# Optimization experiments

Measured on AMD Instinct MI355X. Metric: run time of the kernel, lower is better.

## Reference

```python
import jax, jax.numpy as jnp
import numpy as np

N = 100000
E = 400000
G = 2000  # number of graphs in batch
IN_DIM = 32
H = 192
L = 4
EPS = 1e-5


def setup_inputs() -> dict:
    key = jax.random.key(0)
    ks = jax.random.split(key, 20)
    x = jax.random.normal(ks[0], (N, IN_DIM), jnp.float32)
    edge_src = jax.random.randint(ks[1], (E,), 0, N, jnp.int32)
    edge_dst = jax.random.randint(ks[2], (E,), 0, N, jnp.int32)
    batch = jnp.sort(jax.random.randint(ks[3], (N,), 0, G, jnp.int32))
    s_in = 1.0 / np.sqrt(IN_DIM)
    s_h = 1.0 / np.sqrt(H)
    return {
        "x": x,
        "edge_src": edge_src,
        "edge_dst": edge_dst,
        "batch": batch,
        # layer 0 (in_dim -> H); weights stored [in, out]
        "Wrel0": jax.random.uniform(ks[4], (IN_DIM, H), jnp.float32, -s_in, s_in),
        "brel0": jax.random.uniform(ks[5], (H,), jnp.float32, -s_in, s_in),
        "Wroot0": jax.random.uniform(ks[6], (IN_DIM, H), jnp.float32, -s_in, s_in),
        # layers 1..3 stacked (H -> H)
        "Wrel": jax.random.uniform(ks[7], (L - 1, H, H), jnp.float32, -s_h, s_h),
        "brel": jax.random.uniform(ks[8], (L - 1, H), jnp.float32, -s_h, s_h),
        "Wroot": jax.random.uniform(ks[9], (L - 1, H, H), jnp.float32, -s_h, s_h),
        # batchnorm affine params for all 4 layers
        "gamma": jnp.ones((L, H), jnp.float32),
        "beta": jnp.zeros((L, H), jnp.float32),
        # head MLP and output
        "Wh1": jax.random.uniform(ks[10], (H, H), jnp.float32, -s_h, s_h),
        "bh1": jax.random.uniform(ks[11], (H,), jnp.float32, -s_h, s_h),
        "Wh2": jax.random.uniform(ks[12], (H, H), jnp.float32, -s_h, s_h),
        "bh2": jax.random.uniform(ks[13], (H,), jnp.float32, -s_h, s_h),
        "Wout": jax.random.uniform(ks[14], (H, 1), jnp.float32, -s_h, s_h),
        "bout": jax.random.uniform(ks[15], (1,), jnp.float32, -s_h, s_h),
    }


def _rel_conv(x, edge_src, edge_dst, Wrel, brel, Wroot):
    # message: lin_rel(x_j); applying the linear at node level first is the
    # same math as per-edge (linear commutes with gather) and cheaper.
    h = x @ Wrel + brel                      # [N, out]
    agg = jax.ops.segment_sum(h[edge_src], edge_dst, num_segments=N)
    return agg + x @ Wroot


def _bn_relu(h, g, b):
    # BatchNorm1d in training mode: batch stats over node dim, biased var
    mu = h.mean(axis=0)
    var = jnp.var(h, axis=0)
    h = (h - mu) * jax.lax.rsqrt(var + EPS) * g + b
    return jax.nn.relu(h)


def reference(x, edge_src, edge_dst, batch, Wrel0, brel0, Wroot0,
              Wrel, brel, Wroot, gamma, beta, Wh1, bh1, Wh2, bh2, Wout, bout):
    h = _bn_relu(_rel_conv(x, edge_src, edge_dst, Wrel0, brel0, Wroot0),
                 gamma[0], beta[0])
    for i in range(L - 1):
        h = _bn_relu(_rel_conv(h, edge_src, edge_dst, Wrel[i], brel[i], Wroot[i]),
                     gamma[i + 1], beta[i + 1])
    # global mean pool over graphs
    sums = jax.ops.segment_sum(h, batch, num_segments=G)          # [G, H]
    cnt = jax.ops.segment_sum(jnp.ones((N,), h.dtype), batch, num_segments=G)
    g = sums / jnp.maximum(cnt, 1.0)[:, None]
    # head MLP (dropout is identity at eval) + output linear
    g = jax.nn.relu(g @ Wh1 + bh1) @ Wh2 + bh2
    return g @ Wout + bout                                        # [G, 1]
```

## Files before the change

kernel.cpp:

```cpp
#include <hip/hip_runtime.h>

#define HDIM 192
#define EPS 1e-5f

typedef __attribute__((ext_vector_type(8))) _Float16 half8;
typedef __attribute__((ext_vector_type(4))) float floatx4;

__device__ __forceinline__ float h2f(ushort u) {
    union { ushort u; _Float16 h; } c; c.u = u; return (float)c.h;
}
__device__ __forceinline__ ushort f2h(float x) {
    _Float16 h = (_Float16)x;
    union { _Float16 h; ushort u; } c; c.h = h; return c.u;
}
__device__ __forceinline__ uint4 pack8(const ushort* h) {
    uint4 p;
    p.x = h[0] | ((uint)h[1] << 16); p.y = h[2] | ((uint)h[3] << 16);
    p.z = h[4] | ((uint)h[5] << 16); p.w = h[6] | ((uint)h[7] << 16);
    return p;
}

__device__ __forceinline__ void gload_lds16(const ushort* g, ushort* l) {
    __builtin_amdgcn_global_load_lds(
        (const __attribute__((address_space(1))) unsigned int*)g,
        (__attribute__((address_space(3))) unsigned int*)l, 16, 0, 0);
}

#define WAITV0() asm volatile("s_waitcnt vmcnt(0)" ::: "memory")


struct PrepArgs {
    const float* src[6];
    ushort*      dst[6];
    int K[6];
    int off[7];
};

__global__ __launch_bounds__(256) void prep_all_k(PrepArgs a)
{
    int idx = blockIdx.x * 256 + threadIdx.x;
    if (idx >= a.off[6]) return;
    int i = 0;
    #pragma unroll
    for (int t = 1; t < 6; ++t) if (idx >= a.off[t]) i = t;
    int r = idx - a.off[i];
    int K = a.K[i];
    int perMat = (K >> 5) * 12 * 64;
    int mat = r / perMat;
    r -= mat * perMat;
    int lane = r & 63;
    int ct = (r >> 6) % 12;
    int kc = r / (12 * 64);
    int col = ct * 16 + (lane & 15);
    int kb  = kc * 32 + (lane >> 4) * 8;
    const float* Wm = a.src[i] + (size_t)mat * K * HDIM;
    ushort* base = a.dst[i] + (size_t)mat * K * HDIM;
    size_t o = (size_t)kc * 6144 + (size_t)(ct * 64 + lane) * 8;
    #pragma unroll
    for (int j = 0; j < 8; ++j)
        base[o + j] = f2h(Wm[(size_t)(kb + j) * HDIM + col]);
}

__global__ __launch_bounds__(256) void conv_half_k(
    const float* __restrict__ src, ushort* __restrict__ dst, int R, int C)
{
    int OC = C >> 3;
    int idx = blockIdx.x * 256 + threadIdx.x;
    if (idx >= R * OC) return;
    int r = idx / OC;
    int o = idx - r * OC;
    float4 v0 = ((const float4*)(src + (size_t)r * C + o * 8))[0];
    float4 v1 = ((const float4*)(src + (size_t)r * C + o * 8))[1];
    float v[8] = {v0.x, v0.y, v0.z, v0.w, v1.x, v1.y, v1.z, v1.w};
    ushort h[8];
    #pragma unroll
    for (int t = 0; t < 8; ++t) h[t] = f2h(v[t]);
    *(uint4*)(dst + (size_t)r * C + o * 8) = pack8(h);
}

template<bool DUAL, bool RELU, bool DEG, bool STATS, int NKC>
__global__ __launch_bounds__(256, 3) void gemm_mfma_k(
    const ushort* __restrict__ A1h, const ushort* __restrict__ W1f,
    const ushort* __restrict__ A2h, const ushort* __restrict__ W2f,
    const float* __restrict__ degf, const float* __restrict__ bias,
    ushort* __restrict__ C, float* __restrict__ pstats, int N, int K)
{
    constexpr int KR   = NKC * 32;
    constexpr int RS   = KR + 8;
    constexpr int SLAB = 64 * RS;
    constexpr int NINSTR = SLAB / 512;
    constexpr int NCH  = DUAL ? 2 * NKC : NKC;
    constexpr int SMEMU = ((DUAL ? 2 * SLAB : SLAB) > 12800)
                            ? (DUAL ? 2 * SLAB : SLAB) : 12800;

    __shared__ float sstat[2][HDIM];
    __shared__ __align__(16) ushort smem[SMEMU];
    const int tid  = threadIdx.x;
    const int wave = tid >> 6;
    const int lane = tid & 63;
    const int row0 = blockIdx.x * 64;
    const int m16 = lane & 15;
    const int g4  = lane >> 4;

    if (STATS && tid < HDIM) { sstat[0][tid] = 0.f; sstat[1][tid] = 0.f; }

    auto stage = [&](const ushort* Ab, int slabOff) {
        #pragma unroll
        for (int i = wave; i < NINSTR; i += 4) {
            int slotB = i * 1024 + lane * 16;
            int r   = slotB / (RS * 2);
            int off = slotB - r * (RS * 2);
            if (off >= KR * 2) off = KR * 2 - 16;
            int rr = row0 + r; if (rr >= N) rr = N - 1;
            gload_lds16(Ab + (size_t)rr * KR + (off >> 1),
                        smem + slabOff + i * 512);
        }
    };

    stage(A1h, 0);
    if constexpr (DUAL) stage(A2h, SLAB);
    WAITV0();
    __builtin_amdgcn_s_barrier();
    __builtin_amdgcn_sched_barrier(0);

    auto loadB = [&](int c, half8* b) {
        bool ph = DUAL && (c >= NKC);
        int kc = ph ? c - NKC : c;
        const ushort* Bp = (ph ? W2f : W1f) + (size_t)kc * 6144
                         + (size_t)(wave * 192 + lane) * 8;
        #pragma unroll
        for (int ct = 0; ct < 3; ++ct)
            b[ct] = *(const half8*)(Bp + ct * 512);
    };

    floatx4 acc[4][3];
    #pragma unroll
    for (int s = 0; s < 4; ++s)
        #pragma unroll
        for (int ct = 0; ct < 3; ++ct) acc[s][ct] = (floatx4){0.f, 0.f, 0.f, 0.f};

    half8 bA[3], bB[3];
    loadB(0, bA);
    #pragma unroll
    for (int c = 0; c < NCH; ++c) {
        if (c + 1 < NCH) loadB(c + 1, (c & 1) ? bA : bB);
        const int base = (DUAL && c >= NKC) ? SLAB : 0;
        const int kc   = (DUAL && c >= NKC) ? c - NKC : c;
        const ushort* aB = smem + base + m16 * RS + kc * 32 + g4 * 8;
        half8 a[4];
        #pragma unroll
        for (int s = 0; s < 4; ++s)
            a[s] = *(const half8*)(aB + s * 16 * RS);
        const half8* bu = (c & 1) ? bB : bA;
        #pragma unroll
        for (int ct = 0; ct < 3; ++ct)
            #pragma unroll
            for (int s = 0; s < 4; ++s)
                acc[s][ct] = __builtin_amdgcn_mfma_f32_16x16x32_f16(a[s], bu[ct], acc[s][ct], 0, 0, 0);
    }

    __syncthreads();
    #pragma unroll
    for (int ct = 0; ct < 3; ++ct) {
        int col = wave * 48 + ct * 16 + m16;
        float bv = bias ? bias[col] : 0.f;
        float lsum = 0.f, lsq = 0.f;
        #pragma unroll
        for (int s = 0; s < 4; ++s) {
            #pragma unroll
            for (int reg = 0; reg < 4; ++reg) {
                int rloc = s * 16 + g4 * 4 + reg;
                int rr = row0 + rloc;
                int rrc = rr < N ? rr : N - 1;
                float v = acc[s][ct][reg] + (DEG ? degf[rrc] * bv : bv);
                if (STATS && rr < N) { lsum += v; lsq += v * v; }
                if (RELU) v = fmaxf(v, 0.f);
                smem[rloc * 200 + col] = f2h(v);
            }
        }
        if (STATS) {
            lsum += __shfl_xor(lsum, 16); lsum += __shfl_xor(lsum, 32);
            lsq  += __shfl_xor(lsq, 16);  lsq  += __shfl_xor(lsq, 32);
            if (g4 == 0) {
                atomicAdd(&sstat[0][col], lsum);
                atomicAdd(&sstat[1][col], lsq);
            }
        }
    }
    __syncthreads();
    {
        int rowsLeft = N - row0; if (rowsLeft > 64) rowsLeft = 64;
        int lim = rowsLeft * 24;
        ushort* Cb = C + (size_t)row0 * HDIM;
        #pragma unroll
        for (int k = 0; k < 6; ++k) {
            int u = tid + k * 256;
            if (u < lim) {
                int r  = u / 24;
                int c8 = (u - r * 24) * 8;
                *(uint4*)(Cb + (size_t)u * 8) =
                    *(const uint4*)(smem + r * 200 + c8);
            }
        }
    }
    if (STATS) {
        if (tid < HDIM) {
            float* pb = pstats + (size_t)blockIdx.x * (2 * HDIM);
            pb[tid]        = sstat[0][tid];
            pb[HDIM + tid] = sstat[1][tid];
        }
    }
}

__global__ __launch_bounds__(512, 4) void gemm_fused_k(
    const ushort* __restrict__ Hraw, const ushort* __restrict__ W1f,
    const ushort* __restrict__ W2f,
    const float* __restrict__ degf, const float* __restrict__ bias,
    const float* __restrict__ instats, const float* __restrict__ gammaL,
    const float* __restrict__ betaL, float invN,
    const int* __restrict__ row_ptr, const int* __restrict__ col,
    ushort* __restrict__ C, float* __restrict__ pstats, int N)
{
    constexpr int KR   = 192;
    constexpr int RS   = 200;
    constexpr int SLAB = 64 * RS;
    constexpr int NINSTR = SLAB / 512;
    constexpr int NKC  = 6, NCH = 12;

    __shared__ float sstat[2][HDIM];
    __shared__ __align__(16) ushort smem[2 * SLAB];
    const int tid  = threadIdx.x;
    const int wave = tid >> 6;
    const int lane = tid & 63;
    const int row0 = blockIdx.x * 64;
    const int m16 = lane & 15;
    const int g4  = lane >> 4;

    #pragma unroll
    for (int i = wave; i < NINSTR; i += 8) {
        int slotB = i * 1024 + lane * 16;
        int r   = slotB / (RS * 2);
        int off = slotB - r * (RS * 2);
        if (off >= KR * 2) off = KR * 2 - 16;
        int rr = row0 + r; if (rr >= N) rr = N - 1;
        gload_lds16(Hraw + (size_t)rr * KR + (off >> 1),
                    smem + SLAB + i * 512);
    }
    WAITV0();
    __builtin_amdgcn_s_barrier();
    __builtin_amdgcn_sched_barrier(0);

    if (tid < HDIM) {
        float mu  = instats[tid] * invN;
        float var = instats[HDIM + tid] * invN - mu * mu;
        float s = gammaL[tid] * rsqrtf(var + EPS);
        sstat[0][tid] = s;
        sstat[1][tid] = betaL[tid] - mu * s;
    }
    __syncthreads();

    const int r  = tid >> 3;
    const int q8 = tid & 7;
    {
        ushort* rowp = smem + SLAB + r * RS + q8 * 24;
        #pragma unroll
        for (int k = 0; k < 3; ++k) {
            uint4 hv = *(uint4*)(rowp + k * 8);
            uint hu[4] = {hv.x, hv.y, hv.z, hv.w};
            ushort oh[8];
            #pragma unroll
            for (int e = 0; e < 4; ++e) {
                int ch = q8 * 24 + k * 8 + e * 2;
                float v0 = h2f((ushort)(hu[e] & 0xffffu)) * sstat[0][ch]     + sstat[1][ch];
                float v1 = h2f((ushort)(hu[e] >> 16))     * sstat[0][ch + 1] + sstat[1][ch + 1];
                oh[2*e]   = f2h(fmaxf(v0, 0.f));
                oh[2*e+1] = f2h(fmaxf(v1, 0.f));
            }
            *(uint4*)(rowp + k * 8) = pack8(oh);
        }
    }
    {
        float acc[24];
        #pragma unroll
        for (int i = 0; i < 24; ++i) acc[i] = 0.f;
        int rr = row0 + r;
        if (rr < N) {
            int j0 = row_ptr[rr], j1 = row_ptr[rr + 1];
            const ushort* hp = Hraw + q8 * 24;
            for (int j = j0; j < j1; ++j) {
                int s = col[j];
                const ushort* rp = hp + (size_t)s * KR;
                uint4 h0 = *(const uint4*)(rp);
                uint4 h1 = *(const uint4*)(rp + 8);
                uint4 h2 = *(const uint4*)(rp + 16);
                uint hu[12] = {h0.x,h0.y,h0.z,h0.w, h1.x,h1.y,h1.z,h1.w,
                               h2.x,h2.y,h2.z,h2.w};
                #pragma unroll
                for (int e = 0; e < 12; ++e) {
                    int ch = q8 * 24 + e * 2;
                    float v0 = h2f((ushort)(hu[e] & 0xffffu)) * sstat[0][ch]     + sstat[1][ch];
                    float v1 = h2f((ushort)(hu[e] >> 16))     * sstat[0][ch + 1] + sstat[1][ch + 1];
                    acc[e*2]     += fmaxf(v0, 0.f);
                    acc[e*2 + 1] += fmaxf(v1, 0.f);
                }
            }
        }
        ushort* dst = smem + r * RS + q8 * 24;
        #pragma unroll
        for (int ck = 0; ck < 3; ++ck) {
            ushort oh[8];
            #pragma unroll
            for (int e = 0; e < 8; ++e) oh[e] = f2h(acc[ck*8 + e]);
            *(uint4*)(dst + ck * 8) = pack8(oh);
        }
    }
    __syncthreads();
    if (tid < HDIM) { sstat[0][tid] = 0.f; sstat[1][tid] = 0.f; }

    const int rg = wave >> 2;
    const int cg = wave & 3;

    auto loadB = [&](int c, half8* b) {
        bool ph = (c >= NKC);
        int kc = ph ? c - NKC : c;
        const ushort* Bp = (ph ? W2f : W1f) + (size_t)kc * 6144
                         + (size_t)(cg * 192 + lane) * 8;
        #pragma unroll
        for (int ct = 0; ct < 3; ++ct)
            b[ct] = *(const half8*)(Bp + ct * 512);
    };

    floatx4 acc[2][3];
    #pragma unroll
    for (int s = 0; s < 2; ++s)
        #pragma unroll
        for (int ct = 0; ct < 3; ++ct) acc[s][ct] = (floatx4){0.f, 0.f, 0.f, 0.f};

    half8 bA[3], bB[3];
    loadB(0, bA);
    #pragma unroll
    for (int c = 0; c < NCH; ++c) {
        if (c + 1 < NCH) loadB(c + 1, (c & 1) ? bA : bB);
        const int base = (c >= NKC) ? SLAB : 0;
        const int kc   = (c >= NKC) ? c - NKC : c;
        const ushort* aB = smem + base + (rg * 32 + m16) * RS + kc * 32 + g4 * 8;
        half8 a[2];
        #pragma unroll
        for (int s = 0; s < 2; ++s)
            a[s] = *(const half8*)(aB + s * 16 * RS);
        const half8* bu = (c & 1) ? bB : bA;
        #pragma unroll
        for (int ct = 0; ct < 3; ++ct)
            #pragma unroll
            for (int s = 0; s < 2; ++s)
                acc[s][ct] = __builtin_amdgcn_mfma_f32_16x16x32_f16(a[s], bu[ct], acc[s][ct], 0, 0, 0);
    }

    __syncthreads();
    #pragma unroll
    for (int ct = 0; ct < 3; ++ct) {
        int colc = cg * 48 + ct * 16 + m16;
        float bv = bias[colc];
        float lsum = 0.f, lsq = 0.f;
        #pragma unroll
        for (int s = 0; s < 2; ++s) {
            #pragma unroll
            for (int reg = 0; reg < 4; ++reg) {
                int rloc = rg * 32 + s * 16 + g4 * 4 + reg;
                int rr = row0 + rloc;
                int rrc = rr < N ? rr : N - 1;
                float v = acc[s][ct][reg] + degf[rrc] * bv;
                if (rr < N) { lsum += v; lsq += v * v; }
                smem[rloc * 200 + colc] = f2h(v);
            }
        }
        lsum += __shfl_xor(lsum, 16); lsum += __shfl_xor(lsum, 32);
        lsq  += __shfl_xor(lsq, 16);  lsq  += __shfl_xor(lsq, 32);
        if (g4 == 0) {
            atomicAdd(&sstat[0][colc], lsum);
            atomicAdd(&sstat[1][colc], lsq);
        }
    }
    __syncthreads();
    {
        int rowsLeft = N - row0; if (rowsLeft > 64) rowsLeft = 64;
        int lim = rowsLeft * 24;
        ushort* Cb = C + (size_t)row0 * HDIM;
        #pragma unroll
        for (int k = 0; k < 3; ++k) {
            int u = tid + k * 512;
            if (u < lim) {
                int rr = u / 24;
                int c8 = (u - rr * 24) * 8;
                *(uint4*)(Cb + (size_t)u * 8) =
                    *(const uint4*)(smem + rr * 200 + c8);
            }
        }
    }
    if (tid < HDIM) {
        float* pb = pstats + (size_t)blockIdx.x * (2 * HDIM);
        pb[tid]        = sstat[0][tid];
        pb[HDIM + tid] = sstat[1][tid];
    }
}

__global__ __launch_bounds__(256) void bn_reduce_k(
    const float* __restrict__ pbuf, float* __restrict__ stats, int nb)
{
    __shared__ float red[32][9];
    int t  = threadIdx.x;
    int cl = t & 7;
    int s  = t >> 3;
    int c  = blockIdx.x * 8 + cl;
    float acc = 0.f;
    int b = s;
    for (; b + 96 < nb; b += 128) {
        float a0 = pbuf[(size_t)b * 384 + c];
        float a1 = pbuf[(size_t)(b + 32) * 384 + c];
        float a2 = pbuf[(size_t)(b + 64) * 384 + c];
        float a3 = pbuf[(size_t)(b + 96) * 384 + c];
        acc += a0 + a1 + a2 + a3;
    }
    for (; b < nb; b += 32)
        acc += pbuf[(size_t)b * 384 + c];
    red[s][cl] = acc;
    __syncthreads();
    if (t < 8) {
        float a = 0.f;
        #pragma unroll
        for (int i = 0; i < 32; ++i) a += red[i][t];
        stats[blockIdx.x * 8 + t] = a;
    }
}

__global__ __launch_bounds__(256) void hist_k(
    const int* __restrict__ dst, int* __restrict__ deg, int E)
{
    int e = blockIdx.x * 256 + threadIdx.x;
    if (e < E) atomicAdd(&deg[dst[e]], 1);
}

__global__ __launch_bounds__(256) void block_sum_k(
    const int* __restrict__ deg, int* __restrict__ bsum, int N)
{
    __shared__ int s[256];
    int t = threadIdx.x;
    int n = blockIdx.x * 256 + t;
    s[t] = (n < N) ? deg[n] : 0;
    __syncthreads();
    for (int off = 128; off > 0; off >>= 1) {
        if (t < off) s[t] += s[t + off];
        __syncthreads();
    }
    if (t == 0) bsum[blockIdx.x] = s[0];
}

__global__ __launch_bounds__(512) void scan_bsum_k(int* __restrict__ bsum, int nb)
{
    __shared__ int s[512];
    int t = threadIdx.x;
    int v = (t < nb) ? bsum[t] : 0;
    s[t] = v;
    __syncthreads();
    for (int off = 1; off < 512; off <<= 1) {
        int u = (t >= off) ? s[t - off] : 0;
        __syncthreads();
        s[t] += u;
        __syncthreads();
    }
    if (t < nb) bsum[t] = s[t] - v;
}

__global__ __launch_bounds__(256) void row_ptr_k(
    const int* __restrict__ deg, const int* __restrict__ bsum,
    int* __restrict__ row_ptr, int* __restrict__ cursor,
    float* __restrict__ degf, int N, int E)
{
    __shared__ int s[256];
    int t = threadIdx.x;
    int n = blockIdx.x * 256 + t;
    int v = (n < N) ? deg[n] : 0;
    s[t] = v;
    __syncthreads();
    for (int off = 1; off < 256; off <<= 1) {
        int u = (t >= off) ? s[t - off] : 0;
        __syncthreads();
        s[t] += u;
        __syncthreads();
    }
    int ex = s[t] - v + bsum[blockIdx.x];
    if (n < N) {
        row_ptr[n] = ex;
        cursor[n]  = ex;
        degf[n]    = (float)v;
    }
    if (blockIdx.x == 0 && t == 0) row_ptr[N] = E;
}

__global__ __launch_bounds__(256) void fill_k(
    const int* __restrict__ src, const int* __restrict__ dst,
    int* __restrict__ cursor, int* __restrict__ col, int E)
{
    int e = blockIdx.x * 256 + threadIdx.x;
    if (e < E) {
        int p = atomicAdd(&cursor[dst[e]], 1);
        col[p] = src[e];
    }
}

__global__ __launch_bounds__(256) void gather_h_k(
    const ushort* __restrict__ xh, const int* __restrict__ row_ptr,
    const int* __restrict__ col, ushort* __restrict__ gh, int N, int K)
{
    int OC = K >> 3;
    int idx = blockIdx.x * 256 + threadIdx.x;
    if (idx >= N * OC) return;
    int n = idx / OC;
    int o = idx - n * OC;
    const ushort* hp = xh + o * 8;
    int j0 = row_ptr[n], j1 = row_ptr[n + 1];
    float acc[8] = {0.f,0.f,0.f,0.f,0.f,0.f,0.f,0.f};
    auto addrow = [&](uint4 hv) {
        uint hu[4] = {hv.x, hv.y, hv.z, hv.w};
        #pragma unroll
        for (int t = 0; t < 4; ++t) {
            acc[2*t]   += h2f((ushort)(hu[t] & 0xffffu));
            acc[2*t+1] += h2f((ushort)(hu[t] >> 16));
        }
    };
    int j = j0;
    for (; j + 3 < j1; j += 4) {
        int s0 = col[j], s1 = col[j+1], s2 = col[j+2], s3 = col[j+3];
        uint4 v0 = *(const uint4*)(hp + (size_t)s0 * K);
        uint4 v1 = *(const uint4*)(hp + (size_t)s1 * K);
        uint4 v2 = *(const uint4*)(hp + (size_t)s2 * K);
        uint4 v3 = *(const uint4*)(hp + (size_t)s3 * K);
        addrow(v0); addrow(v1); addrow(v2); addrow(v3);
    }
    for (; j < j1; ++j)
        addrow(*(const uint4*)(hp + (size_t)col[j] * K));
    ushort oh[8];
    #pragma unroll
    for (int t = 0; t < 8; ++t) oh[t] = f2h(acc[t]);
    *(uint4*)(gh + (size_t)n * K + o * 8) = pack8(oh);
}

__global__ __launch_bounds__(192) void pool_bn_k(
    const ushort* __restrict__ h, const float* __restrict__ stats,
    const float* __restrict__ gamma, const float* __restrict__ beta,
    float invN, const int* __restrict__ batch,
    ushort* __restrict__ gsh, int G, int N)
{
    __shared__ int bounds[2];
    int g = blockIdx.x;
    int c = threadIdx.x;
    if (c < 2) {
        int key = g + c;
        int lo = 0, hi = N;
        while (lo < hi) {
            int mid = (lo + hi) >> 1;
            if (batch[mid] < key) lo = mid + 1; else hi = mid;
        }
        bounds[c] = lo;
    }
    __syncthreads();
    int r0 = bounds[0], r1 = bounds[1];
    float mu  = stats[c] * invN;
    float var = stats[HDIM + c] * invN - mu * mu;
    float sc  = gamma[c] * rsqrtf(var + EPS);
    float sh  = beta[c] - mu * sc;
    const ushort* base = h + c;
    float s = 0.f;
    for (int r = r0; r < r1; ++r)
        s += fmaxf(h2f(base[(size_t)r * HDIM]) * sc + sh, 0.f);
    float m = s / fmaxf((float)(r1 - r0), 1.f);
    gsh[(size_t)g * HDIM + c] = f2h(m);
}

__global__ __launch_bounds__(64) void out_dot_k(
    const ushort* __restrict__ g2h, const float* __restrict__ Wout,
    const float* __restrict__ bout, float* __restrict__ out, int G)
{
    int gi = blockIdx.x;
    int t = threadIdx.x;
    float s = 0.f;
    #pragma unroll
    for (int j = 0; j < 3; ++j) {
        int c = t + j * 64;
        s += h2f(g2h[(size_t)gi * HDIM + c]) * Wout[c];
    }
    #pragma unroll
    for (int off = 32; off > 0; off >>= 1) s += __shfl_down(s, off, 64);
    if (t == 0) out[gi] = s + bout[0];
}

extern "C" void kernel_launch(void* const* d_in, const int* in_sizes, int n_in,
                              void* d_out, int out_size, void* d_ws, size_t ws_size,
                              hipStream_t stream)
{
    const float* x      = (const float*)d_in[0];
    const int*   esrc   = (const int*)d_in[1];
    const int*   edst   = (const int*)d_in[2];
    const int*   batch  = (const int*)d_in[3];
    const float* Wrel0  = (const float*)d_in[4];
    const float* brel0  = (const float*)d_in[5];
    const float* Wroot0 = (const float*)d_in[6];
    const float* Wrel   = (const float*)d_in[7];
    const float* brel   = (const float*)d_in[8];
    const float* Wroot  = (const float*)d_in[9];
    const float* gamma  = (const float*)d_in[10];
    const float* beta   = (const float*)d_in[11];
    const float* Wh1    = (const float*)d_in[12];
    const float* bh1    = (const float*)d_in[13];
    const float* Wh2    = (const float*)d_in[14];
    const float* bh2    = (const float*)d_in[15];
    const float* Wout   = (const float*)d_in[16];
    const float* bout   = (const float*)d_in[17];
    float* out = (float*)d_out;

    const int N  = in_sizes[3];
    const int E  = in_sizes[1];
    const int K0 = in_sizes[0] / N;
    const int G  = out_size;
    const int nBlocks = (N + 255) / 256;
    const float invN = 1.0f / (float)N;

    char* p = (char*)d_ws;
    auto carve = [&](size_t bytes) -> void* {
        void* r = (void*)p; p += (bytes + 255) & ~(size_t)255; return r;
    };
    ushort* bufa_h= (ushort*)carve((size_t)N * HDIM * 2);
    ushort* bufb_h= (ushort*)carve((size_t)N * HDIM * 2);
    ushort* xh    = (ushort*)carve((size_t)N * K0 * 2);
    ushort* gh    = (ushort*)carve((size_t)N * K0 * 2);
    ushort* gsh   = (ushort*)carve((size_t)G * HDIM * 2);
    ushort* g1h   = (ushort*)carve((size_t)G * HDIM * 2);
    ushort* g2h   = (ushort*)carve((size_t)G * HDIM * 2);
    int*    deg   = (int*)   carve((size_t)N * 4);
    float*  bnsums= (float*) carve(4 * 2 * HDIM * 4);
    size_t  zspan = (char*)(bnsums + 4 * 2 * HDIM) - (char*)deg;
    float*  degf  = (float*) carve((size_t)N * 4);
    int*    row_ptr=(int*)   carve((size_t)(N + 1) * 4);
    int*    cursor= (int*)   carve((size_t)N * 4);
    int*    col   = (int*)   carve((size_t)E * 4);
    int*    bsum  = (int*)   carve((size_t)nBlocks * 4);
    ushort* Wrel0f= (ushort*)carve((size_t)K0 * HDIM * 2);
    ushort* Wroot0f=(ushort*)carve((size_t)K0 * HDIM * 2);
    ushort* Wrelf = (ushort*)carve((size_t)3 * HDIM * HDIM * 2);
    ushort* Wrootf= (ushort*)carve((size_t)3 * HDIM * HDIM * 2);
    ushort* Wh1f  = (ushort*)carve((size_t)HDIM * HDIM * 2);
    ushort* Wh2f  = (ushort*)carve((size_t)HDIM * HDIM * 2);

    dim3 b256(256);
    const int eBlocks = (E + 255) / 256;
    const int gemmN = (N + 63) / 64;
    const int gemmG = (G + 63) / 64;

    float*  pbuf  = (float*) carve((size_t)gemmN * 2 * HDIM * 4);

    {
        PrepArgs a;
        int t0 = (K0 >> 5) * 12 * 64;
        int t1 = (HDIM >> 5) * 12 * 64;
        a.src[0] = Wrel0;  a.dst[0] = Wrel0f;  a.K[0] = K0;
        a.src[1] = Wroot0; a.dst[1] = Wroot0f; a.K[1] = K0;
        a.src[2] = Wrel;   a.dst[2] = Wrelf;   a.K[2] = HDIM;
        a.src[3] = Wroot;  a.dst[3] = Wrootf;  a.K[3] = HDIM;
        a.src[4] = Wh1;    a.dst[4] = Wh1f;    a.K[4] = HDIM;
        a.src[5] = Wh2;    a.dst[5] = Wh2f;    a.K[5] = HDIM;
        a.off[0] = 0;
        a.off[1] = a.off[0] + t0;
        a.off[2] = a.off[1] + t0;
        a.off[3] = a.off[2] + 3 * t1;
        a.off[4] = a.off[3] + 3 * t1;
        a.off[5] = a.off[4] + t1;
        a.off[6] = a.off[5] + t1;
        prep_all_k<<<(a.off[6] + 255) / 256, b256, 0, stream>>>(a);
    }
    conv_half_k<<<((N * (K0 >> 3)) + 255) / 256, b256, 0, stream>>>(x, xh, N, K0);

    hipMemsetAsync(deg, 0, zspan, stream);
    hist_k<<<eBlocks, b256, 0, stream>>>(edst, deg, E);
    block_sum_k<<<nBlocks, b256, 0, stream>>>(deg, bsum, N);
    scan_bsum_k<<<1, dim3(512), 0, stream>>>(bsum, nBlocks);
    row_ptr_k<<<nBlocks, b256, 0, stream>>>(deg, bsum, row_ptr, cursor, degf, N, E);
    fill_k<<<eBlocks, b256, 0, stream>>>(esrc, edst, cursor, col, E);

    gather_h_k<<<((N * (K0 >> 3)) + 255) / 256, b256, 0, stream>>>(
        xh, row_ptr, col, gh, N, K0);
    gemm_mfma_k<true, false, true, true, 1><<<gemmN, b256, 0, stream>>>(
        gh, Wrel0f, xh, Wroot0f, degf, brel0, bufa_h, pbuf, N, K0);
    bn_reduce_k<<<48, b256, 0, stream>>>(pbuf, bnsums, gemmN);

    ushort* rd = bufa_h;
    ushort* wr = bufb_h;
    for (int l = 1; l < 4; ++l) {
        const ushort* Wrf = Wrelf  + (size_t)(l - 1) * HDIM * HDIM;
        const ushort* Wtf = Wrootf + (size_t)(l - 1) * HDIM * HDIM;
        const float*  br  = brel   + (size_t)(l - 1) * HDIM;
        const float*  st  = bnsums + (size_t)(l - 1) * 2 * HDIM;
        const float*  gm  = gamma  + (size_t)(l - 1) * HDIM;
        const float*  bt  = beta   + (size_t)(l - 1) * HDIM;
        gemm_fused_k<<<gemmN, dim3(512), 0, stream>>>(
            rd, Wrf, Wtf, degf, br, st, gm, bt, invN,
            row_ptr, col, wr, pbuf, N);
        bn_reduce_k<<<48, b256, 0, stream>>>(pbuf, bnsums + l * 2 * HDIM, gemmN);
        ushort* tmp = rd; rd = wr; wr = tmp;
    }

    pool_bn_k<<<G, dim3(192), 0, stream>>>(
        rd, bnsums + 3 * 2 * HDIM, gamma + 3 * HDIM, beta + 3 * HDIM,
        invN, batch, gsh, G, N);

    gemm_mfma_k<false, true, false, false, 6><<<gemmG, b256, 0, stream>>>(
        gsh, Wh1f, nullptr, nullptr, nullptr, bh1, g1h, nullptr, G, HDIM);
    gemm_mfma_k<false, false, false, false, 6><<<gemmG, b256, 0, stream>>>(
        g1h, Wh2f, nullptr, nullptr, nullptr, bh2, g2h, nullptr, G, HDIM);
    out_dot_k<<<G, dim3(64), 0, stream>>>(g2h, Wout, bout, out, G);
}
```

Measured before the change: 447.4 us.

## Halve LDS in fused GEMM by running root pass before aggregation

The fused layer kernel used to keep two 64x200 fp16 slabs in shared memory, one for the aggregated neighbours and one for the normalised self rows. It now keeps a single slab: the root-weight GEMM runs first on the normalised self rows, then the same buffer is reused for the neighbour aggregation before the relation-weight GEMM accumulates into the same registers. The launch-bounds hint rises from 4 to 8 blocks per CU. The stats prologue also now overlaps the async global-to-LDS load. The extra barrier between phases and the higher register pressure from the occupancy hint may cost some of the benefit.

```diff
diff --git a/kernel.cpp b/kernel.cpp
--- a/kernel.cpp
+++ b/kernel.cpp
@@ -212,7 +212,7 @@
     }
 }
 
-__global__ __launch_bounds__(512, 4) void gemm_fused_k(
+__global__ __launch_bounds__(512, 8) void gemm_fused_k(
     const ushort* __restrict__ Hraw, const ushort* __restrict__ W1f,
     const ushort* __restrict__ W2f,
     const float* __restrict__ degf, const float* __restrict__ bias,
@@ -225,10 +225,10 @@
     constexpr int RS   = 200;
     constexpr int SLAB = 64 * RS;
     constexpr int NINSTR = SLAB / 512;
-    constexpr int NKC  = 6, NCH = 12;
+    constexpr int NKC  = 6;
 
     __shared__ float sstat[2][HDIM];
-    __shared__ __align__(16) ushort smem[2 * SLAB];
+    __shared__ __align__(16) ushort smem[SLAB];
     const int tid  = threadIdx.x;
     const int wave = tid >> 6;
     const int lane = tid & 63;
@@ -244,12 +244,8 @@
         if (off >= KR * 2) off = KR * 2 - 16;
         int rr = row0 + r; if (rr >= N) rr = N - 1;
         gload_lds16(Hraw + (size_t)rr * KR + (off >> 1),
-                    smem + SLAB + i * 512);
-    }
-    WAITV0();
-    __builtin_amdgcn_s_barrier();
-    __builtin_amdgcn_sched_barrier(0);
-
+                    smem + i * 512);
+    }
     if (tid < HDIM) {
         float mu  = instats[tid] * invN;
         float var = instats[HDIM + tid] * invN - mu * mu;
@@ -257,12 +253,13 @@
         sstat[0][tid] = s;
         sstat[1][tid] = betaL[tid] - mu * s;
     }
+    WAITV0();
     __syncthreads();
 
     const int r  = tid >> 3;
     const int q8 = tid & 7;
     {
-        ushort* rowp = smem + SLAB + r * RS + q8 * 24;
+        ushort* rowp = smem + r * RS + q8 * 24;
         #pragma unroll
         for (int k = 0; k < 3; ++k) {
             uint4 hv = *(uint4*)(rowp + k * 8);
@@ -279,10 +276,52 @@
             *(uint4*)(rowp + k * 8) = pack8(oh);
         }
     }
+    __syncthreads();
+
+    const int rg = wave >> 2;
+    const int cg = wave & 3;
+
+    auto loadB = [&](const ushort* Wf, int kc, half8* b) {
+        const ushort* Bp = Wf + (size_t)kc * 6144
+                         + (size_t)(cg * 192 + lane) * 8;
+        #pragma unroll
+        for (int ct = 0; ct < 3; ++ct)
+            b[ct] = *(const half8*)(Bp + ct * 512);
+    };
+
+    floatx4 acc[2][3];
+    #pragma unroll
+    for (int s = 0; s < 2; ++s)
+        #pragma unroll
+        for (int ct = 0; ct < 3; ++ct) acc[s][ct] = (floatx4){0.f, 0.f, 0.f, 0.f};
+
+    auto gemmPass = [&](const ushort* Wf) {
+        half8 bA[3], bB[3];
+        loadB(Wf, 0, bA);
+        #pragma unroll
+        for (int kc = 0; kc < NKC; ++kc) {
+            if (kc + 1 < NKC) loadB(Wf, kc + 1, (kc & 1) ? bA : bB);
+            const ushort* aB = smem + (rg * 32 + m16) * RS + kc * 32 + g4 * 8;
+            half8 a[2];
+            #pragma unroll
+            for (int s = 0; s < 2; ++s)
+                a[s] = *(const half8*)(aB + s * 16 * RS);
+            const half8* bu = (kc & 1) ? bB : bA;
+            #pragma unroll
+            for (int ct = 0; ct < 3; ++ct)
+                #pragma unroll
+                for (int s = 0; s < 2; ++s)
+                    acc[s][ct] = __builtin_amdgcn_mfma_f32_16x16x32_f16(a[s], bu[ct], acc[s][ct], 0, 0, 0);
+        }
+    };
+
+    gemmPass(W2f);
+    __syncthreads();
+
     {
-        float acc[24];
-        #pragma unroll
-        for (int i = 0; i < 24; ++i) acc[i] = 0.f;
+        float acg[24];
+        #pragma unroll
+        for (int i = 0; i < 24; ++i) acg[i] = 0.f;
         int rr = row0 + r;
         if (rr < N) {
             int j0 = row_ptr[rr], j1 = row_ptr[rr + 1];
@@ -300,8 +339,8 @@
                     int ch = q8 * 24 + e * 2;
                     float v0 = h2f((ushort)(hu[e] & 0xffffu)) * sstat[0][ch]     + sstat[1][ch];
                     float v1 = h2f((ushort)(hu[e] >> 16))     * sstat[0][ch + 1] + sstat[1][ch + 1];
-                    acc[e*2]     += fmaxf(v0, 0.f);
-                    acc[e*2 + 1] += fmaxf(v1, 0.f);
+                    acg[e*2]     += fmaxf(v0, 0.f);
+                    acg[e*2 + 1] += fmaxf(v1, 0.f);
                 }
             }
         }
@@ -310,51 +349,14 @@
         for (int ck = 0; ck < 3; ++ck) {
             ushort oh[8];
             #pragma unroll
-            for (int e = 0; e < 8; ++e) oh[e] = f2h(acc[ck*8 + e]);
+            for (int e = 0; e < 8; ++e) oh[e] = f2h(acg[ck*8 + e]);
             *(uint4*)(dst + ck * 8) = pack8(oh);
         }
     }
     __syncthreads();
     if (tid < HDIM) { sstat[0][tid] = 0.f; sstat[1][tid] = 0.f; }
 
-    const int rg = wave >> 2;
-    const int cg = wave & 3;
-
-    auto loadB = [&](int c, half8* b) {
-        bool ph = (c >= NKC);
-        int kc = ph ? c - NKC : c;
-        const ushort* Bp = (ph ? W2f : W1f) + (size_t)kc * 6144
-                         + (size_t)(cg * 192 + lane) * 8;
-        #pragma unroll
-        for (int ct = 0; ct < 3; ++ct)
-            b[ct] = *(const half8*)(Bp + ct * 512);
-    };
-
-    floatx4 acc[2][3];
-    #pragma unroll
-    for (int s = 0; s < 2; ++s)
-        #pragma unroll
-        for (int ct = 0; ct < 3; ++ct) acc[s][ct] = (floatx4){0.f, 0.f, 0.f, 0.f};
-
-    half8 bA[3], bB[3];
-    loadB(0, bA);
-    #pragma unroll
-    for (int c = 0; c < NCH; ++c) {
-        if (c + 1 < NCH) loadB(c + 1, (c & 1) ? bA : bB);
-        const int base = (c >= NKC) ? SLAB : 0;
-        const int kc   = (c >= NKC) ? c - NKC : c;
-        const ushort* aB = smem + base + (rg * 32 + m16) * RS + kc * 32 + g4 * 8;
-        half8 a[2];
-        #pragma unroll
-        for (int s = 0; s < 2; ++s)
-            a[s] = *(const half8*)(aB + s * 16 * RS);
-        const half8* bu = (c & 1) ? bB : bA;
-        #pragma unroll
-        for (int ct = 0; ct < 3; ++ct)
-            #pragma unroll
-            for (int s = 0; s < 2; ++s)
-                acc[s][ct] = __builtin_amdgcn_mfma_f32_16x16x32_f16(a[s], bu[ct], acc[s][ct], 0, 0, 0);
-    }
+    gemmPass(W1f);
 
     __syncthreads();
     #pragma unroll
```

Result: slower. 844.5 us (+88.7%).
